# Performance work log

Hardware: AMD Instinct MI355X
Metric: run time of the kernel (lower is better)

Reference implementation:

```python
import jax, jax.numpy as jnp
import numpy as np

K = 256        # top-k positions kept along the sparse (sequence) axis
GROUPS = 16    # number of channel groups
P = 2          # Lp norm order
EPS = 1e-9


def setup_inputs() -> dict:
    key = jax.random.key(0)
    x = jax.random.normal(key, (32, 2048, 1024), dtype=jnp.float32)
    return {"x": x}


def reference(x):
    B, S, C = x.shape              # batch, sparse axis (seq), group axis (channels)
    g = GROUPS
    gs = C // g                    # channels per group
    # group-wise Lp norm: (B, S, g)
    xg = x.reshape(B, S, g, gs)
    norms = jnp.power(jnp.sum(jnp.power(jnp.abs(xg), P), axis=-1) + EPS, 1.0 / P)
    # topk along the sparse axis per (batch, group)
    norms_t = norms.transpose(0, 2, 1).reshape(B * g, S)   # (B*g, S)
    _, idx = jax.lax.top_k(norms_t, K)                      # (B*g, K)
    # scatter binary mask at topk positions
    rows = jnp.arange(B * g, dtype=jnp.int32)[:, None]
    mask = jnp.zeros((B * g, S), dtype=x.dtype).at[rows, idx].set(1.0)
    mask = mask.reshape(B, g, S).transpose(0, 2, 1)         # (B, S, g)
    # broadcast mask over channels within each group and multiply
    out = (mask[:, :, :, None] * xg).reshape(B, S, C)
    return out
```

## Files before the change

### kernel.cpp

```cpp
#include <hip/hip_runtime.h>


#define BB 32
#define SS 2048
#define CC 1024
#define GG 16
#define KTOP 256

__device__ inline double shfl_xor_dbl(double v, int m) {
  union {
    double d;
    int i[2];
  } u;
  u.d = v;
  u.i[0] = __shfl_xor(u.i[0], m, 64);
  u.i[1] = __shfl_xor(u.i[1], m, 64);
  return u.d;
}

__global__ __launch_bounds__(512) void gsa_fused(const float4* __restrict__ x4,
                                                 float4* __restrict__ out4) {
  __shared__ float norm[SS];
  __shared__ unsigned long long Tsh;
  const int t = threadIdx.x;
  const int lane16 = t & 15;
  const int srow = t >> 4;
  const int b = blockIdx.x >> 4;
  const int g = blockIdx.x & 15;
  const size_t bbase = (size_t)b * SS;
  const int chunk = g * 16 + lane16;

  for (int it = 0; it < SS / 32; ++it) {
    const int s = it * 32 + srow;
    float4 v = x4[(bbase + s) * 256 + chunk];
    double d = (double)v.x * v.x + (double)v.y * v.y + (double)v.z * v.z +
               (double)v.w * v.w;
    d += shfl_xor_dbl(d, 1);
    d += shfl_xor_dbl(d, 2);
    d += shfl_xor_dbl(d, 4);
    d += shfl_xor_dbl(d, 8);
    if (lane16 == 0) norm[s] = sqrtf(__fadd_rn((float)d, 1e-9f));
  }
  __syncthreads();

  if (t < 64) {
    unsigned long long key[32];
#pragma unroll
    for (int j = 0; j < 32; ++j) {
      const int s = j * 64 + t;
      key[j] = ((unsigned long long)__float_as_uint(norm[s]) << 11) |
               (unsigned)(SS - 1 - s);
    }
    unsigned long long T = 0ULL;
    for (int bit = 41; bit >= 0; --bit) {
      unsigned long long cand = T | (1ULL << bit);
      int local = 0;
#pragma unroll
      for (int j = 0; j < 32; ++j) local += (key[j] >= cand) ? 1 : 0;
      for (int m = 32; m >= 1; m >>= 1) local += __shfl_xor(local, m, 64);
      if (local >= KTOP) T = cand;
    }
    if (t == 0) Tsh = T;
  }
  __syncthreads();
  const unsigned long long T = Tsh;

  for (int it = 0; it < SS / 32; ++it) {
    const int s = it * 32 + srow;
    const unsigned long long key =
        ((unsigned long long)__float_as_uint(norm[s]) << 11) |
        (unsigned)(SS - 1 - s);
    float4 v = make_float4(0.f, 0.f, 0.f, 0.f);
    if (key >= T) v = x4[(bbase + s) * 256 + chunk];
    out4[(bbase + s) * 256 + chunk] = v;
  }
}

extern "C" void kernel_launch(void* const* d_in, const int* in_sizes, int n_in,
                              void* d_out, int out_size, void* d_ws, size_t ws_size,
                              hipStream_t stream) {
  const float* x = (const float*)d_in[0];
  float* out = (float*)d_out;
  gsa_fused<<<BB * GG, 512, 0, stream>>>((const float4*)x, (float4*)out);
}
```

Measured before the change: 484.7 us.

## Split fused kernel into norm, select and masked-write kernels

Replaces the single fused kernel, which ran one block per (batch, group) with strided 256-byte row segments, with three kernels. The first computes group norms over full contiguous rows into workspace, the second finds a threshold per (batch, group) with one wavefront each, and the third writes the masked output with nontemporal stores. This gives much higher parallelism and fully coalesced row access than the 512 blocks of the original. In exchange it re-reads x in the write pass, adds two extra launches and small workspace traffic, and falls back to the fused kernel when no workspace is provided.

```diff
diff --git a/kernel.cpp b/kernel.cpp
--- a/kernel.cpp
+++ b/kernel.cpp
@@ -6,6 +6,9 @@
 #define CC 1024
 #define GG 16
 #define KTOP 256
+#define ROWS 8
+
+typedef float f32x4 __attribute__((ext_vector_type(4)));
 
 __device__ inline double shfl_xor_dbl(double v, int m) {
   union {
@@ -16,6 +19,89 @@
   u.i[0] = __shfl_xor(u.i[0], m, 64);
   u.i[1] = __shfl_xor(u.i[1], m, 64);
   return u.d;
+}
+
+__global__ __launch_bounds__(256) void gsa_norms(const float4* __restrict__ x4,
+                                                 float* __restrict__ nrm) {
+  const int t = threadIdx.x;
+  const int lane16 = t & 15;
+  const int g = t >> 4;
+  const size_t base = (size_t)blockIdx.x * ROWS;
+
+  float4 vv[ROWS];
+#pragma unroll
+  for (int r = 0; r < ROWS; ++r) vv[r] = x4[(base + r) * 256 + t];
+
+#pragma unroll
+  for (int r = 0; r < ROWS; ++r) {
+    const float4 v = vv[r];
+    double d = (double)v.x * v.x + (double)v.y * v.y + (double)v.z * v.z +
+               (double)v.w * v.w;
+    d += shfl_xor_dbl(d, 1);
+    d += shfl_xor_dbl(d, 2);
+    d += shfl_xor_dbl(d, 4);
+    d += shfl_xor_dbl(d, 8);
+    if (lane16 == 0) {
+      const size_t row = base + r;
+      const int b = (int)(row >> 11);
+      const int s = (int)(row & (SS - 1));
+      nrm[((size_t)(b * GG + g) << 11) | s] = sqrtf(__fadd_rn((float)d, 1e-9f));
+    }
+  }
+}
+
+__global__ __launch_bounds__(64) void gsa_select(
+    const float* __restrict__ nrm, unsigned long long* __restrict__ Tarr) {
+  const int row = blockIdx.x;
+  const int t = threadIdx.x;
+  unsigned long long key[SS / 64];
+#pragma unroll
+  for (int j = 0; j < SS / 64; ++j) {
+    const int s = j * 64 + t;
+    key[j] =
+        ((unsigned long long)__float_as_uint(nrm[((size_t)row << 11) | s])
+         << 11) |
+        (unsigned)(SS - 1 - s);
+  }
+  unsigned long long T = 0ULL;
+  for (int bit = 41; bit >= 0; --bit) {
+    const unsigned long long cand = T | (1ULL << bit);
+    int local = 0;
+#pragma unroll
+    for (int j = 0; j < SS / 64; ++j) local += (key[j] >= cand) ? 1 : 0;
+    for (int m = 32; m >= 1; m >>= 1) local += __shfl_xor(local, m, 64);
+    if (local >= KTOP) T = cand;
+  }
+  if (t == 0) Tarr[row] = T;
+}
+
+__global__ __launch_bounds__(256) void gsa_write(
+    const float4* __restrict__ x4, const float* __restrict__ nrm,
+    const unsigned long long* __restrict__ Tarr, float4* __restrict__ out4) {
+  const int t = threadIdx.x;
+  const int g = t >> 4;
+  const size_t base = (size_t)blockIdx.x * ROWS;
+  const int b = (int)(base >> 11);
+  const int s0 = (int)(base & (SS - 1));
+  const unsigned long long T = Tarr[b * GG + g];
+
+  float4 v[ROWS];
+#pragma unroll
+  for (int r = 0; r < ROWS; ++r) {
+    const int s = s0 + r;
+    const unsigned long long key =
+        ((unsigned long long)__float_as_uint(
+             nrm[((size_t)(b * GG + g) << 11) | s])
+         << 11) |
+        (unsigned)(SS - 1 - s);
+    v[r] = make_float4(0.f, 0.f, 0.f, 0.f);
+    if (key >= T) v[r] = x4[(base + r) * 256 + t];
+  }
+#pragma unroll
+  for (int r = 0; r < ROWS; ++r) {
+    __builtin_nontemporal_store(*(const f32x4*)&v[r],
+                                (f32x4*)(out4 + (base + r) * 256 + t));
+  }
 }
 
 __global__ __launch_bounds__(512) void gsa_fused(const float4* __restrict__ x4,
@@ -77,9 +163,20 @@
 }
 
 extern "C" void kernel_launch(void* const* d_in, const int* in_sizes, int n_in,
-                              void* d_out, int out_size, void* d_ws, size_t ws_size,
-                              hipStream_t stream) {
-  const float* x = (const float*)d_in[0];
-  float* out = (float*)d_out;
-  gsa_fused<<<BB * GG, 512, 0, stream>>>((const float4*)x, (float4*)out);
+                              void* d_out, int out_size, void* d_ws,
+                              size_t ws_size, hipStream_t stream) {
+  const float4* x4 = (const float4*)d_in[0];
+  float4* out4 = (float4*)d_out;
+  const size_t nrm_bytes = (size_t)BB * GG * SS * sizeof(float);
+  const size_t need = nrm_bytes + (size_t)BB * GG * sizeof(unsigned long long);
+  if (d_ws != nullptr && ws_size >= need) {
+    float* nrm = (float*)d_ws;
+    unsigned long long* Tarr =
+        (unsigned long long*)((char*)d_ws + nrm_bytes);
+    gsa_norms<<<BB * SS / ROWS, 256, 0, stream>>>(x4, nrm);
+    gsa_select<<<BB * GG, 64, 0, stream>>>(nrm, Tarr);
+    gsa_write<<<BB * SS / ROWS, 256, 0, stream>>>(x4, nrm, Tarr, out4);
+  } else {
+    gsa_fused<<<BB * GG, 512, 0, stream>>>(x4, out4);
+  }
 }
```

Measured after the change: 473.5 us. 2.3% less time.

## Double block size, unroll row loops, ballot-based radix select, nontemporal stores

Applied to the files above, without the earlier changes.

Raises the block size to 1024 threads and processes two rows per iteration, so each thread has more loads in flight. The top-k threshold search now keeps 32-bit norm bits and counts matches with wave ballots and popcount instead of 64-bit key compares plus shuffle reductions. Output is written with nontemporal stores to avoid polluting the cache. The larger block adds register pressure, and the launch_bounds occupancy hint may not be achievable.

```diff
diff --git a/kernel.cpp b/kernel.cpp
--- a/kernel.cpp
+++ b/kernel.cpp
@@ -3,9 +3,10 @@
 
 #define BB 32
 #define SS 2048
-#define CC 1024
 #define GG 16
 #define KTOP 256
+
+typedef float f32x4 __attribute__((ext_vector_type(4)));
 
 __device__ inline double shfl_xor_dbl(double v, int m) {
   union {
@@ -18,10 +19,11 @@
   return u.d;
 }
 
-__global__ __launch_bounds__(512) void gsa_fused(const float4* __restrict__ x4,
-                                                 float4* __restrict__ out4) {
+__global__ __launch_bounds__(1024, 8) void gsa_fused3(
+    const float4* __restrict__ x4, float4* __restrict__ out4) {
   __shared__ float norm[SS];
-  __shared__ unsigned long long Tsh;
+  __shared__ unsigned int Tch_sh;
+  __shared__ int Tscl_sh;
   const int t = threadIdx.x;
   const int lane16 = t & 15;
   const int srow = t >> 4;
@@ -30,56 +32,79 @@
   const size_t bbase = (size_t)b * SS;
   const int chunk = g * 16 + lane16;
 
-  for (int it = 0; it < SS / 32; ++it) {
-    const int s = it * 32 + srow;
-    float4 v = x4[(bbase + s) * 256 + chunk];
-    double d = (double)v.x * v.x + (double)v.y * v.y + (double)v.z * v.z +
-               (double)v.w * v.w;
-    d += shfl_xor_dbl(d, 1);
-    d += shfl_xor_dbl(d, 2);
-    d += shfl_xor_dbl(d, 4);
-    d += shfl_xor_dbl(d, 8);
-    if (lane16 == 0) norm[s] = sqrtf(__fadd_rn((float)d, 1e-9f));
+  for (int it = 0; it < 16; ++it) {
+    const int s0 = it * 128 + srow;
+    const int s1 = s0 + 64;
+    const float4 va = x4[(bbase + s0) * 256 + chunk];
+    const float4 vb = x4[(bbase + s1) * 256 + chunk];
+    double da = (double)va.x * va.x + (double)va.y * va.y +
+                (double)va.z * va.z + (double)va.w * va.w;
+    double db = (double)vb.x * vb.x + (double)vb.y * vb.y +
+                (double)vb.z * vb.z + (double)vb.w * vb.w;
+    da += shfl_xor_dbl(da, 1);
+    db += shfl_xor_dbl(db, 1);
+    da += shfl_xor_dbl(da, 2);
+    db += shfl_xor_dbl(db, 2);
+    da += shfl_xor_dbl(da, 4);
+    db += shfl_xor_dbl(db, 4);
+    da += shfl_xor_dbl(da, 8);
+    db += shfl_xor_dbl(db, 8);
+    if (lane16 == 0) {
+      norm[s0] = sqrtf(__fadd_rn((float)da, 1e-9f));
+      norm[s1] = sqrtf(__fadd_rn((float)db, 1e-9f));
+    }
   }
   __syncthreads();
 
   if (t < 64) {
-    unsigned long long key[32];
+    unsigned int nb[32];
 #pragma unroll
-    for (int j = 0; j < 32; ++j) {
-      const int s = j * 64 + t;
-      key[j] = ((unsigned long long)__float_as_uint(norm[s]) << 11) |
-               (unsigned)(SS - 1 - s);
-    }
+    for (int j = 0; j < 32; ++j) nb[j] = __float_as_uint(norm[j * 64 + t]);
     unsigned long long T = 0ULL;
     for (int bit = 41; bit >= 0; --bit) {
-      unsigned long long cand = T | (1ULL << bit);
-      int local = 0;
+      const unsigned long long cand = T | (1ULL << bit);
+      const unsigned int ch = (unsigned int)(cand >> 11);
+      const int scl = 2047 - (int)(cand & 2047ULL);
+      int cnt = 0;
 #pragma unroll
-      for (int j = 0; j < 32; ++j) local += (key[j] >= cand) ? 1 : 0;
-      for (int m = 32; m >= 1; m >>= 1) local += __shfl_xor(local, m, 64);
-      if (local >= KTOP) T = cand;
+      for (int j = 0; j < 32; ++j) {
+        const bool pred =
+            (nb[j] > ch) | ((nb[j] == ch) & ((t + j * 64) <= scl));
+        cnt += (int)__popcll(__ballot(pred));
+      }
+      if (cnt >= KTOP) T = cand;
     }
-    if (t == 0) Tsh = T;
+    if (t == 0) {
+      Tch_sh = (unsigned int)(T >> 11);
+      Tscl_sh = 2047 - (int)(T & 2047ULL);
+    }
   }
   __syncthreads();
-  const unsigned long long T = Tsh;
+  const unsigned int ch = Tch_sh;
+  const int scl = Tscl_sh;
 
-  for (int it = 0; it < SS / 32; ++it) {
-    const int s = it * 32 + srow;
-    const unsigned long long key =
-        ((unsigned long long)__float_as_uint(norm[s]) << 11) |
-        (unsigned)(SS - 1 - s);
-    float4 v = make_float4(0.f, 0.f, 0.f, 0.f);
-    if (key >= T) v = x4[(bbase + s) * 256 + chunk];
-    out4[(bbase + s) * 256 + chunk] = v;
+  for (int it = 0; it < 16; ++it) {
+    const int s0 = it * 128 + srow;
+    const int s1 = s0 + 64;
+    const unsigned int n0 = __float_as_uint(norm[s0]);
+    const unsigned int n1 = __float_as_uint(norm[s1]);
+    const bool sel0 = (n0 > ch) | ((n0 == ch) & (s0 <= scl));
+    const bool sel1 = (n1 > ch) | ((n1 == ch) & (s1 <= scl));
+    float4 v0 = make_float4(0.f, 0.f, 0.f, 0.f);
+    float4 v1 = make_float4(0.f, 0.f, 0.f, 0.f);
+    if (sel0) v0 = x4[(bbase + s0) * 256 + chunk];
+    if (sel1) v1 = x4[(bbase + s1) * 256 + chunk];
+    __builtin_nontemporal_store(*(const f32x4*)&v0,
+                                (f32x4*)(out4 + (bbase + s0) * 256 + chunk));
+    __builtin_nontemporal_store(*(const f32x4*)&v1,
+                                (f32x4*)(out4 + (bbase + s1) * 256 + chunk));
   }
 }
 
 extern "C" void kernel_launch(void* const* d_in, const int* in_sizes, int n_in,
-                              void* d_out, int out_size, void* d_ws, size_t ws_size,
-                              hipStream_t stream) {
-  const float* x = (const float*)d_in[0];
-  float* out = (float*)d_out;
-  gsa_fused<<<BB * GG, 512, 0, stream>>>((const float4*)x, (float4*)out);
+                              void* d_out, int out_size, void* d_ws,
+                              size_t ws_size, hipStream_t stream) {
+  const float4* x4 = (const float4*)d_in[0];
+  float4* out4 = (float4*)d_out;
+  gsa_fused3<<<BB * GG, 1024, 0, stream>>>(x4, out4);
 }
```

Measured after the change: 473.5 us. -2.3%, faster.
